# Performance work log

Hardware: AMD Instinct MI355X
Metric: run time of the kernel (lower is better)

Reference implementation:

```python
import jax, jax.numpy as jnp
import numpy as np

EMBED = 1024
HEADS = 16
HEAD_DIM = EMBED // HEADS


def setup_inputs() -> dict:
    key = jax.random.key(0)
    ks = jax.random.split(key, 12)
    N, S, E = 4, 2048, EMBED
    scale = 1.0 / np.sqrt(E)
    inp = {
        "values": jax.random.normal(ks[0], (N, S, E), dtype=jnp.float32),
        "keys": jax.random.normal(ks[1], (N, S, E), dtype=jnp.float32),
        "query": jax.random.normal(ks[2], (N, S, E), dtype=jnp.float32),
        "mask": jnp.ones((N, 1, 1, S), dtype=jnp.int32),
        # Linear params: y = x @ W + b (W stored as [in, out])
        "Wv": jax.random.normal(ks[3], (E, E), dtype=jnp.float32) * scale,
        "bv": jnp.zeros((E,), dtype=jnp.float32),
        "Wk": jax.random.normal(ks[4], (E, E), dtype=jnp.float32) * scale,
        "bk": jnp.zeros((E,), dtype=jnp.float32),
        "Wq": jax.random.normal(ks[5], (E, E), dtype=jnp.float32) * scale,
        "bq": jnp.zeros((E,), dtype=jnp.float32),
        "Wo": jax.random.normal(ks[6], (E, E), dtype=jnp.float32) * scale,
        "bo": jnp.zeros((E,), dtype=jnp.float32),
    }
    return inp


def reference(values, keys, query, mask, Wv, bv, Wk, bk, Wq, bq, Wo, bo):
    N, Q, E = query.shape
    V = values.shape[1]
    K = keys.shape[1]
    v = (values @ Wv + bv).reshape(N, V, HEADS, HEAD_DIM)
    k = (keys @ Wk + bk).reshape(N, K, HEADS, HEAD_DIM)
    q = (query @ Wq + bq).reshape(N, Q, HEADS, HEAD_DIM)
    # energy: [N, H, Q, K]
    energy = jnp.einsum("nqhd,nkhd->nhqk", q, k)
    energy = jnp.where(mask == 0, jnp.float32(-1e20), energy)
    # NOTE: original scales by sqrt(embed_size), not sqrt(head_dim)
    attn = jax.nn.softmax(energy / jnp.sqrt(jnp.float32(E)), axis=3)
    out = jnp.einsum("nhql,nlhd->nqhd", attn, v).reshape(N, Q, E)
    return out @ Wo + bo
```

## Files before the change

### kernel.cpp

```cpp
#include <hip/hip_runtime.h>

#define H 16
#define DH 64
#define S 2048
#define E 1024
#define NB 4

typedef short short8_t __attribute__((ext_vector_type(8)));
typedef float float4_t __attribute__((ext_vector_type(4)));

__device__ inline unsigned short f2bf(float f) {
    union { float f; unsigned u; } v; v.f = f;
    unsigned r = v.u + 0x7fffu + ((v.u >> 16) & 1u);
    return (unsigned short)(r >> 16);
}

__device__ __forceinline__ unsigned pk_bf16(float a, float b) {
    union { float f; unsigned u; } ua, ub;
    ua.f = a; ub.f = b;
    unsigned ra = ua.u + 0x7fffu + ((ua.u >> 16) & 1u);
    unsigned rb = ub.u + 0x7fffu + ((ub.u >> 16) & 1u);
    return __builtin_amdgcn_perm(rb, ra, 0x07060302u);
}

__device__ __forceinline__ void async_copy16(const unsigned short* g, unsigned short* l) {
    __builtin_amdgcn_global_load_lds(
        (const __attribute__((address_space(1))) unsigned int*)g,
        (__attribute__((address_space(3))) unsigned int*)l, 16, 0, 0);
}

__global__ __launch_bounds__(256) void xcvt_kernel(
    const float* __restrict__ v, const float* __restrict__ k,
    const float* __restrict__ q, unsigned short* __restrict__ xv,
    unsigned short* __restrict__ xk, unsigned short* __restrict__ xq)
{
    const int z = blockIdx.y;
    const float* src = (z == 0) ? v : (z == 1) ? k : q;
    unsigned short* dst = (z == 0) ? xv : (z == 1) ? xk : xq;
    size_t i0 = ((size_t)blockIdx.x * 256 + threadIdx.x) * 8;
    float4 f0 = *reinterpret_cast<const float4*>(src + i0);
    float4 f1 = *reinterpret_cast<const float4*>(src + i0 + 4);
    uint4 o;
    o.x = pk_bf16(f0.x, f0.y); o.y = pk_bf16(f0.z, f0.w);
    o.z = pk_bf16(f1.x, f1.y); o.w = pk_bf16(f1.z, f1.w);
    *reinterpret_cast<uint4*>(dst + i0) = o;
}

__global__ __launch_bounds__(256) void wcvt_kernel(
    const float* __restrict__ Wv, const float* __restrict__ Wk,
    const float* __restrict__ Wq, const float* __restrict__ Wo,
    unsigned short* __restrict__ Wt)
{
    __shared__ float tile[64][65];
    const float* W = (blockIdx.z == 0) ? Wv : (blockIdx.z == 1) ? Wk
                   : (blockIdx.z == 2) ? Wq : Wo;
    unsigned short* out = Wt + (size_t)blockIdx.z * (E * E);
    const int k0 = blockIdx.x * 64, n0 = blockIdx.y * 64;
    const int tid = threadIdx.x;
#pragma unroll
    for (int i = 0; i < 4; ++i) {
        int c = i * 256 + tid;
        int kl = c >> 4, nl4 = (c & 15) * 4;
        float4 v = *reinterpret_cast<const float4*>(W + (size_t)(k0 + kl) * E + n0 + nl4);
        tile[kl][nl4 + 0] = v.x; tile[kl][nl4 + 1] = v.y;
        tile[kl][nl4 + 2] = v.z; tile[kl][nl4 + 3] = v.w;
    }
    __syncthreads();
#pragma unroll
    for (int i = 0; i < 4; ++i) {
        int c = i * 256 + tid;
        int nl = c >> 4, kl4 = (c & 15) * 4;
        ushort4 o;
        o.x = f2bf(tile[kl4 + 0][nl]); o.y = f2bf(tile[kl4 + 1][nl]);
        o.z = f2bf(tile[kl4 + 2][nl]); o.w = f2bf(tile[kl4 + 3][nl]);
        *reinterpret_cast<ushort4*>(out + (size_t)(n0 + nl) * E + k0 + kl4) = o;
    }
}

__global__ __launch_bounds__(256) void proj_kernel(
    const unsigned short* __restrict__ A, const unsigned short* __restrict__ WT,
    const float* __restrict__ bias, unsigned short* __restrict__ out, int mode)
{
    __shared__ __align__(16) unsigned short As[2][128][64];
    __shared__ __align__(16) unsigned short Bs[2][128][64];

    const int tid = threadIdx.x;
    const int m0 = blockIdx.y * 128;
    const int n0 = blockIdx.x * 128;
    const int wave = tid >> 6, lane = tid & 63;
    const int wm = wave >> 1, wn = wave & 1;
    const int quad = lane >> 4, l16 = lane & 15;
    const int r8 = lane >> 3;
    const int c8 = (lane & 7) ^ (r8 & 7);

    float4_t acc[4][4];
#pragma unroll
    for (int i = 0; i < 4; ++i)
#pragma unroll
        for (int j = 0; j < 4; ++j) { float4_t z = {0.f,0.f,0.f,0.f}; acc[i][j] = z; }

#pragma unroll
    for (int j = 0; j < 4; ++j) {
        int row = wave * 32 + j * 8 + r8;
        async_copy16(A  + (size_t)(m0 + row) * E + c8 * 8, &As[0][wave * 32 + j * 8][0]);
        async_copy16(WT + (size_t)(n0 + row) * E + c8 * 8, &Bs[0][wave * 32 + j * 8][0]);
    }

    for (int it = 0; it < 16; ++it) {
        const int cur = it & 1, nxt = cur ^ 1;
        __syncthreads();

        if (it < 15) {
            const int kn = (it + 1) * 64;
#pragma unroll
            for (int j = 0; j < 4; ++j) {
                int row = wave * 32 + j * 8 + r8;
                async_copy16(A  + (size_t)(m0 + row) * E + kn + c8 * 8, &As[nxt][wave * 32 + j * 8][0]);
                async_copy16(WT + (size_t)(n0 + row) * E + kn + c8 * 8, &Bs[nxt][wave * 32 + j * 8][0]);
            }
        }
#pragma unroll
        for (int kk = 0; kk < 2; ++kk) {
            short8_t a[4], b[4];
#pragma unroll
            for (int mi = 0; mi < 4; ++mi)
                a[mi] = *reinterpret_cast<const short8_t*>(
                    &As[cur][wm * 64 + mi * 16 + l16][((kk * 4 + quad) ^ (l16 & 7)) * 8]);
#pragma unroll
            for (int nj = 0; nj < 4; ++nj)
                b[nj] = *reinterpret_cast<const short8_t*>(
                    &Bs[cur][wn * 64 + nj * 16 + l16][((kk * 4 + quad) ^ (l16 & 7)) * 8]);
#pragma unroll
            for (int mi = 0; mi < 4; ++mi)
#pragma unroll
                for (int nj = 0; nj < 4; ++nj)
                    acc[mi][nj] = __builtin_amdgcn_mfma_f32_16x16x32_bf16(a[mi], b[nj], acc[mi][nj], 0, 0, 0);
        }
    }
#pragma unroll
    for (int mi = 0; mi < 4; ++mi) {
#pragma unroll
        for (int nj = 0; nj < 4; ++nj) {
            int gcol = n0 + wn * 64 + nj * 16 + l16;
            float bvv = bias[gcol];
            int h = gcol >> 6, d = gcol & 63;
#pragma unroll
            for (int r = 0; r < 4; ++r) {
                int gm = m0 + wm * 64 + mi * 16 + quad * 4 + r;
                float val = acc[mi][nj][r] + bvv;
                int n = gm >> 11, s = gm & 2047;
                size_t addr;
                if (mode == 0)
                    addr = (((size_t)(n * H + h)) * DH + d) * S + s;
                else
                    addr = (((size_t)(n * H + h)) * S + s) * DH + d;
                out[addr] = f2bf(val);
            }
        }
    }
}

__global__ __launch_bounds__(256) void flash_kernel(
    const unsigned short* __restrict__ Qb, const unsigned short* __restrict__ Kb,
    const unsigned short* __restrict__ VTb, const int* __restrict__ mask,
    unsigned short* __restrict__ AO)
{
    __shared__ __align__(16) unsigned short Ks[2][64][64];
    __shared__ __align__(16) unsigned short Vs[2][64][64];
    __shared__ __align__(16) unsigned short Ps[4][32][72];
    __shared__ float am[2][64];
    __shared__ float lbuf[4][32];

    const int tid = threadIdx.x;
    const int wave = tid >> 6, lane = tid & 63;
    const int quad = lane >> 4, l16 = lane & 15;
    const int r8 = lane >> 3;
    const int c8 = (lane & 7) ^ (r8 & 7);
    const int qt = blockIdx.x;
    const int nh = blockIdx.y;
    const int n = nh >> 4, h = nh & 15;
    const size_t hb = (size_t)nh * S * DH;
    const unsigned short* Qh = Qb + hb;
    const unsigned short* Kh = Kb + hb;
    const unsigned short* Vh = VTb + hb;
    const int* mp = mask + n * S;

    const float c1 = 0.03125f * 1.4426950408889634f;
    const float C2_UNMASK = -23.083120654223414f;
    const float C2_MASK   = -1.44e20f;

    short8_t qa[2][2];
#pragma unroll
    for (int qb2 = 0; qb2 < 2; ++qb2)
#pragma unroll
        for (int kk = 0; kk < 2; ++kk) {
            int row = qt * 128 + wave * 32 + qb2 * 16 + l16;
            qa[qb2][kk] = *reinterpret_cast<const short8_t*>(Qh + (size_t)row * DH + kk * 32 + quad * 8);
        }

    float4_t o[2][4];
#pragma unroll
    for (int mi = 0; mi < 2; ++mi)
#pragma unroll
        for (int nj = 0; nj < 4; ++nj) { float4_t z = {0.f,0.f,0.f,0.f}; o[mi][nj] = z; }
    float lsum[2] = {0.f, 0.f};

#pragma unroll
    for (int j = 0; j < 2; ++j) {
        int row = wave * 16 + j * 8 + r8;
        async_copy16(Kh + (size_t)row * DH + c8 * 8, &Ks[0][wave * 16 + j * 8][0]);
        async_copy16(Vh + (size_t)row * S + c8 * 8,  &Vs[0][wave * 16 + j * 8][0]);
    }
    if (tid < 64) am[0][tid] = (mp[tid] == 0) ? C2_MASK : C2_UNMASK;

    for (int it = 0; it < 32; ++it) {
        const int cur = it & 1, nxt = cur ^ 1;
        __syncthreads();

        const int kn = (it < 31) ? (it + 1) * 64 : 0;
#pragma unroll
        for (int j = 0; j < 2; ++j) {
            int row = wave * 16 + j * 8 + r8;
            async_copy16(Kh + (size_t)(kn + row) * DH + c8 * 8, &Ks[nxt][wave * 16 + j * 8][0]);
            async_copy16(Vh + (size_t)row * S + kn + c8 * 8,    &Vs[nxt][wave * 16 + j * 8][0]);
        }
        if (tid < 64) am[nxt][tid] = (mp[kn + tid] == 0) ? C2_MASK : C2_UNMASK;

        float4_t st[4][2];
#pragma unroll
        for (int kvb = 0; kvb < 4; ++kvb)
#pragma unroll
            for (int qb2 = 0; qb2 < 2; ++qb2) { float4_t z = {0.f,0.f,0.f,0.f}; st[kvb][qb2] = z; }
#pragma unroll
        for (int kk = 0; kk < 2; ++kk) {
            short8_t ak[4];
#pragma unroll
            for (int kvb = 0; kvb < 4; ++kvb)
                ak[kvb] = *reinterpret_cast<const short8_t*>(
                    &Ks[cur][kvb * 16 + l16][((kk * 4 + quad) ^ (l16 & 7)) * 8]);
#pragma unroll
            for (int kvb = 0; kvb < 4; ++kvb)
#pragma unroll
                for (int qb2 = 0; qb2 < 2; ++qb2)
                    st[kvb][qb2] = __builtin_amdgcn_mfma_f32_16x16x32_bf16(ak[kvb], qa[qb2][kk], st[kvb][qb2], 0, 0, 0);
        }

#pragma unroll
        for (int kvb = 0; kvb < 4; ++kvb) {
            float4 c2v = *reinterpret_cast<const float4*>(&am[cur][kvb * 16 + quad * 4]);
#pragma unroll
            for (int qb2 = 0; qb2 < 2; ++qb2) {
                float p0 = __builtin_amdgcn_exp2f(st[kvb][qb2][0] * c1 + c2v.x);
                float p1 = __builtin_amdgcn_exp2f(st[kvb][qb2][1] * c1 + c2v.y);
                float p2 = __builtin_amdgcn_exp2f(st[kvb][qb2][2] * c1 + c2v.z);
                float p3 = __builtin_amdgcn_exp2f(st[kvb][qb2][3] * c1 + c2v.w);
                lsum[qb2] += (p0 + p1) + (p2 + p3);
                unsigned w0 = pk_bf16(p0, p1);
                unsigned w1 = pk_bf16(p2, p3);
                *reinterpret_cast<uint2*>(&Ps[wave][qb2 * 16 + l16][kvb * 16 + quad * 4]) =
                    make_uint2(w0, w1);
            }
        }

#pragma unroll
        for (int kk = 0; kk < 2; ++kk) {
            short8_t pa[2], vb[4];
#pragma unroll
            for (int mi = 0; mi < 2; ++mi)
                pa[mi] = *reinterpret_cast<const short8_t*>(&Ps[wave][mi * 16 + l16][kk * 32 + quad * 8]);
#pragma unroll
            for (int nj = 0; nj < 4; ++nj)
                vb[nj] = *reinterpret_cast<const short8_t*>(
                    &Vs[cur][nj * 16 + l16][((kk * 4 + quad) ^ (l16 & 7)) * 8]);
#pragma unroll
            for (int mi = 0; mi < 2; ++mi)
#pragma unroll
                for (int nj = 0; nj < 4; ++nj)
                    o[mi][nj] = __builtin_amdgcn_mfma_f32_16x16x32_bf16(pa[mi], vb[nj], o[mi][nj], 0, 0, 0);
        }
    }

    lsum[0] += __shfl_xor(lsum[0], 16); lsum[0] += __shfl_xor(lsum[0], 32);
    lsum[1] += __shfl_xor(lsum[1], 16); lsum[1] += __shfl_xor(lsum[1], 32);
    if (lane < 16) { lbuf[wave][lane] = lsum[0]; lbuf[wave][16 + lane] = lsum[1]; }

#pragma unroll
    for (int mi = 0; mi < 2; ++mi) {
        float4 lv = *reinterpret_cast<const float4*>(&lbuf[wave][mi * 16 + quad * 4]);
#pragma unroll
        for (int r = 0; r < 4; ++r) {
            float invl = __builtin_amdgcn_rcpf(((const float*)&lv)[r]);
            int qrow = qt * 128 + wave * 32 + mi * 16 + quad * 4 + r;
            size_t gm = (size_t)n * S + qrow;
#pragma unroll
            for (int nj = 0; nj < 4; ++nj) {
                int col = h * DH + nj * 16 + l16;
                AO[gm * E + col] = f2bf(o[mi][nj][r] * invl);
            }
        }
    }
}

__global__ __launch_bounds__(256) void ogemm_kernel(
    const unsigned short* __restrict__ A, const unsigned short* __restrict__ WT,
    const float* __restrict__ bias, float* __restrict__ out)
{
    __shared__ __align__(16) unsigned short As[2][128][64];
    __shared__ __align__(16) unsigned short Bs[2][128][64];

    const int tid = threadIdx.x;
    const int m0 = blockIdx.y * 128;
    const int n0 = blockIdx.x * 128;
    const int wave = tid >> 6, lane = tid & 63;
    const int wm = wave >> 1, wn = wave & 1;
    const int quad = lane >> 4, l16 = lane & 15;
    const int r8 = lane >> 3;
    const int c8 = (lane & 7) ^ (r8 & 7);

    float4_t acc[4][4];
#pragma unroll
    for (int i = 0; i < 4; ++i)
#pragma unroll
        for (int j = 0; j < 4; ++j) { float4_t z = {0.f,0.f,0.f,0.f}; acc[i][j] = z; }

#pragma unroll
    for (int j = 0; j < 4; ++j) {
        int row = wave * 32 + j * 8 + r8;
        async_copy16(A  + (size_t)(m0 + row) * E + c8 * 8, &As[0][wave * 32 + j * 8][0]);
        async_copy16(WT + (size_t)(n0 + row) * E + c8 * 8, &Bs[0][wave * 32 + j * 8][0]);
    }

    for (int it = 0; it < 16; ++it) {
        const int cur = it & 1, nxt = cur ^ 1;
        __syncthreads();

        if (it < 15) {
            const int kn = (it + 1) * 64;
#pragma unroll
            for (int j = 0; j < 4; ++j) {
                int row = wave * 32 + j * 8 + r8;
                async_copy16(A  + (size_t)(m0 + row) * E + kn + c8 * 8, &As[nxt][wave * 32 + j * 8][0]);
                async_copy16(WT + (size_t)(n0 + row) * E + kn + c8 * 8, &Bs[nxt][wave * 32 + j * 8][0]);
            }
        }
#pragma unroll
        for (int kk = 0; kk < 2; ++kk) {
            short8_t a[4], b[4];
#pragma unroll
            for (int mi = 0; mi < 4; ++mi)
                a[mi] = *reinterpret_cast<const short8_t*>(
                    &As[cur][wm * 64 + mi * 16 + l16][((kk * 4 + quad) ^ (l16 & 7)) * 8]);
#pragma unroll
            for (int nj = 0; nj < 4; ++nj)
                b[nj] = *reinterpret_cast<const short8_t*>(
                    &Bs[cur][wn * 64 + nj * 16 + l16][((kk * 4 + quad) ^ (l16 & 7)) * 8]);
#pragma unroll
            for (int mi = 0; mi < 4; ++mi)
#pragma unroll
                for (int nj = 0; nj < 4; ++nj)
                    acc[mi][nj] = __builtin_amdgcn_mfma_f32_16x16x32_bf16(a[mi], b[nj], acc[mi][nj], 0, 0, 0);
        }
    }
#pragma unroll
    for (int mi = 0; mi < 4; ++mi)
#pragma unroll
        for (int nj = 0; nj < 4; ++nj) {
            int gcol = n0 + wn * 64 + nj * 16 + l16;
            float bvv = bias[gcol];
#pragma unroll
            for (int r = 0; r < 4; ++r) {
                int gm = m0 + wm * 64 + mi * 16 + quad * 4 + r;
                out[(size_t)gm * E + gcol] = acc[mi][nj][r] + bvv;
            }
        }
}

extern "C" void kernel_launch(void* const* d_in, const int* in_sizes, int n_in,
                              void* d_out, int out_size, void* d_ws, size_t ws_size,
                              hipStream_t stream) {
    const float* values = (const float*)d_in[0];
    const float* keys   = (const float*)d_in[1];
    const float* query  = (const float*)d_in[2];
    const int*   mask   = (const int*)d_in[3];
    const float* Wv = (const float*)d_in[4];  const float* bv = (const float*)d_in[5];
    const float* Wk = (const float*)d_in[6];  const float* bk = (const float*)d_in[7];
    const float* Wq = (const float*)d_in[8];  const float* bq = (const float*)d_in[9];
    const float* Wo = (const float*)d_in[10]; const float* bo = (const float*)d_in[11];
    float* out = (float*)d_out;

    char* ws = (char*)d_ws;
    unsigned short* Wt = (unsigned short*)ws;
    unsigned short* xv = (unsigned short*)(ws + 8388608);
    unsigned short* xk = (unsigned short*)(ws + 25165824);
    unsigned short* xq = (unsigned short*)(ws + 41943040);
    unsigned short* vt = (unsigned short*)(ws + 58720256);
    unsigned short* kb = xv;
    unsigned short* qb = xk;
    unsigned short* ao = xq;

    xcvt_kernel<<<dim3(4096, 3), 256, 0, stream>>>(values, keys, query, xv, xk, xq);
    wcvt_kernel<<<dim3(16, 16, 4), 256, 0, stream>>>(Wv, Wk, Wq, Wo, Wt);
    proj_kernel<<<dim3(8, 64), 256, 0, stream>>>(xv, Wt,           bv, vt, 0);
    proj_kernel<<<dim3(8, 64), 256, 0, stream>>>(xk, Wt + 1048576, bk, kb, 1);
    proj_kernel<<<dim3(8, 64), 256, 0, stream>>>(xq, Wt + 2097152, bq, qb, 1);
    flash_kernel<<<dim3(16, 64), 256, 0, stream>>>(qb, kb, vt, mask, ao);
    ogemm_kernel<<<dim3(8, 64), 256, 0, stream>>>(ao, Wt + 3145728, bo, out);
}
```

Measured before the change: 395.2 us.

## Keep softmax probabilities in registers and feed PV via 16x16x16 MFMA

Removes the per-wave LDS staging buffer for the probability tile. The S accumulator layout is fed directly as the A operand of 16x16x16 bf16 MFMAs, with V reads adjusted to match. It also switches to a hardware packed bf16 convert, adds s_setprio around the MFMA sections, remaps block indices to spread heads across XCDs, and sets a launch-bounds occupancy hint. This cuts LDS writes, reads and round-trip latency per iteration, at the cost of twice as many smaller-K MFMA instructions for the PV product.

```diff
diff --git a/kernel.cpp b/kernel.cpp
--- a/kernel.cpp
+++ b/kernel.cpp
@@ -7,6 +7,7 @@
 #define NB 4
 
 typedef short short8_t __attribute__((ext_vector_type(8)));
+typedef short short4_t __attribute__((ext_vector_type(4)));
 typedef float float4_t __attribute__((ext_vector_type(4)));
 
 __device__ inline unsigned short f2bf(float f) {
@@ -21,6 +22,22 @@
     unsigned ra = ua.u + 0x7fffu + ((ua.u >> 16) & 1u);
     unsigned rb = ub.u + 0x7fffu + ((ub.u >> 16) & 1u);
     return __builtin_amdgcn_perm(rb, ra, 0x07060302u);
+}
+
+__device__ __forceinline__ unsigned cvt_pk_bf16(float a, float b) {
+    unsigned r;
+    asm("v_cvt_pk_bf16_f32 %0, %1, %2" : "=v"(r) : "v"(a), "v"(b));
+    return r;
+}
+
+__device__ __forceinline__ float4_t mfma16x16x16_bf16(short4_t a, short4_t b, float4_t c) {
+#if __has_builtin(__builtin_amdgcn_mfma_f32_16x16x16bf16_1k)
+    return __builtin_amdgcn_mfma_f32_16x16x16bf16_1k(a, b, c, 0, 0, 0);
+#else
+    float4_t d;
+    asm("v_mfma_f32_16x16x16_bf16 %0, %1, %2, %3" : "=v"(d) : "v"(a), "v"(b), "v"(c));
+    return d;
+#endif
 }
 
 __device__ __forceinline__ void async_copy16(const unsigned short* g, unsigned short* l) {
@@ -160,14 +177,13 @@
     }
 }
 
-__global__ __launch_bounds__(256) void flash_kernel(
+__global__ __launch_bounds__(256, 4) void flash_kernel(
     const unsigned short* __restrict__ Qb, const unsigned short* __restrict__ Kb,
     const unsigned short* __restrict__ VTb, const int* __restrict__ mask,
     unsigned short* __restrict__ AO)
 {
     __shared__ __align__(16) unsigned short Ks[2][64][64];
     __shared__ __align__(16) unsigned short Vs[2][64][64];
-    __shared__ __align__(16) unsigned short Ps[4][32][72];
     __shared__ float am[2][64];
     __shared__ float lbuf[4][32];
 
@@ -176,8 +192,11 @@
     const int quad = lane >> 4, l16 = lane & 15;
     const int r8 = lane >> 3;
     const int c8 = (lane & 7) ^ (r8 & 7);
-    const int qt = blockIdx.x;
-    const int nh = blockIdx.y;
+
+    const int wlin = blockIdx.y * 16 + blockIdx.x;
+    const int wid = (wlin & 7) * 128 + (wlin >> 3);
+    const int qt = wid & 15;
+    const int nh = wid >> 4;
     const int n = nh >> 4, h = nh & 15;
     const size_t hb = (size_t)nh * S * DH;
     const unsigned short* Qh = Qb + hb;
@@ -231,6 +250,7 @@
         for (int kvb = 0; kvb < 4; ++kvb)
 #pragma unroll
             for (int qb2 = 0; qb2 < 2; ++qb2) { float4_t z = {0.f,0.f,0.f,0.f}; st[kvb][qb2] = z; }
+        __builtin_amdgcn_s_setprio(1);
 #pragma unroll
         for (int kk = 0; kk < 2; ++kk) {
             short8_t ak[4];
@@ -244,7 +264,9 @@
                 for (int qb2 = 0; qb2 < 2; ++qb2)
                     st[kvb][qb2] = __builtin_amdgcn_mfma_f32_16x16x32_bf16(ak[kvb], qa[qb2][kk], st[kvb][qb2], 0, 0, 0);
         }
-
+        __builtin_amdgcn_s_setprio(0);
+
+        unsigned pw[2][4][2];
 #pragma unroll
         for (int kvb = 0; kvb < 4; ++kvb) {
             float4 c2v = *reinterpret_cast<const float4*>(&am[cur][kvb * 16 + quad * 4]);
@@ -255,29 +277,30 @@
                 float p2 = __builtin_amdgcn_exp2f(st[kvb][qb2][2] * c1 + c2v.z);
                 float p3 = __builtin_amdgcn_exp2f(st[kvb][qb2][3] * c1 + c2v.w);
                 lsum[qb2] += (p0 + p1) + (p2 + p3);
-                unsigned w0 = pk_bf16(p0, p1);
-                unsigned w1 = pk_bf16(p2, p3);
-                *reinterpret_cast<uint2*>(&Ps[wave][qb2 * 16 + l16][kvb * 16 + quad * 4]) =
-                    make_uint2(w0, w1);
-            }
-        }
-
-#pragma unroll
-        for (int kk = 0; kk < 2; ++kk) {
-            short8_t pa[2], vb[4];
-#pragma unroll
-            for (int mi = 0; mi < 2; ++mi)
-                pa[mi] = *reinterpret_cast<const short8_t*>(&Ps[wave][mi * 16 + l16][kk * 32 + quad * 8]);
+                pw[qb2][kvb][0] = cvt_pk_bf16(p0, p1);
+                pw[qb2][kvb][1] = cvt_pk_bf16(p2, p3);
+            }
+        }
+
+        const int vcol = (quad & 1) * 4;
+        __builtin_amdgcn_s_setprio(1);
+#pragma unroll
+        for (int kvb = 0; kvb < 4; ++kvb) {
+            const int vch = ((kvb * 2 + (quad >> 1)) ^ (l16 & 7)) * 8 + vcol;
+            short4_t vb[4];
 #pragma unroll
             for (int nj = 0; nj < 4; ++nj)
-                vb[nj] = *reinterpret_cast<const short8_t*>(
-                    &Vs[cur][nj * 16 + l16][((kk * 4 + quad) ^ (l16 & 7)) * 8]);
-#pragma unroll
-            for (int mi = 0; mi < 2; ++mi)
+                vb[nj] = *reinterpret_cast<const short4_t*>(&Vs[cur][nj * 16 + l16][vch]);
+#pragma unroll
+            for (int mi = 0; mi < 2; ++mi) {
+                union { unsigned u[2]; short4_t s; } pu;
+                pu.u[0] = pw[mi][kvb][0]; pu.u[1] = pw[mi][kvb][1];
 #pragma unroll
                 for (int nj = 0; nj < 4; ++nj)
-                    o[mi][nj] = __builtin_amdgcn_mfma_f32_16x16x32_bf16(pa[mi], vb[nj], o[mi][nj], 0, 0, 0);
-        }
+                    o[mi][nj] = mfma16x16x16_bf16(pu.s, vb[nj], o[mi][nj]);
+            }
+        }
+        __builtin_amdgcn_s_setprio(0);
     }
 
     lsum[0] += __shfl_xor(lsum[0], 16); lsum[0] += __shfl_xor(lsum[0], 32);
```

After: 377.4 us. 4.5% less time.
